# Performance work log

Hardware: AMD Instinct MI355X
Metric: run time of the kernel (lower is better)

Reference implementation:

```python
import jax, jax.numpy as jnp
import numpy as np


def setup_inputs() -> dict:
    key = jax.random.key(0)
    k1, k2, k3, k4 = jax.random.split(key, 4)
    B, N, F_in, F_out = 8, 2048, 256, 128
    h = jax.random.normal(k1, (B, N, F_in), dtype=jnp.float32)
    # fc: Linear(in_features, out_features, bias=False); store as [F_in, F_out]
    W_fc = jax.random.normal(k2, (F_in, F_out), dtype=jnp.float32) * (1.0 / np.sqrt(F_in))
    # attn_fc: Linear(2*F_out, 1, bias=False) -> split into the two additive halves
    a_i = jax.random.normal(k3, (F_out,), dtype=jnp.float32) * (1.0 / np.sqrt(2 * F_out))
    a_j = jax.random.normal(k4, (F_out,), dtype=jnp.float32) * (1.0 / np.sqrt(2 * F_out))
    return {"h": h, "W_fc": W_fc, "a_i": a_i, "a_j": a_j}


def reference(h, W_fc, a_i, a_j):
    # Wh: [B, N, F_out]
    Wh = jnp.einsum("bnf,fo->bno", h, W_fc)
    # attn_fc(cat([Wh_i, Wh_j])) is linear, so it decomposes additively:
    # e[b,i,j] = <Wh[b,i], a_i> + <Wh[b,j], a_j>  -- same math, no N^2*2F tensor
    s_i = Wh @ a_i  # [B, N]
    s_j = Wh @ a_j  # [B, N]
    e = s_i[:, :, None] + s_j[:, None, :]  # [B, N, N]
    alpha = jax.nn.softmax(jax.nn.leaky_relu(e, negative_slope=0.01), axis=-1)
    h_prime = jnp.einsum("bij,bjo->bio", alpha, Wh)  # [B, N, F_out]
    return h_prime
```

## Files before the change

kernel.cpp:

```cpp
#include <hip/hip_runtime.h>
#include <hip/hip_bf16.h>

#define BATCH 8
#define NN 2048
#define FIN 256
#define FOUT 128
#define ROWS (BATCH*NN)
#define NP1 (NN+1)
#define SEGS 128
#define SLEN (NN/SEGS)

typedef __attribute__((ext_vector_type(8))) __bf16 bf16x8;
typedef __attribute__((ext_vector_type(4))) float f32x4;
typedef __attribute__((ext_vector_type(8))) unsigned short ushort8_t;

__device__ __forceinline__ unsigned pack2(float a, float b){
  __hip_bfloat16 x = __float2bfloat16(a), y = __float2bfloat16(b);
  unsigned short ux = *(unsigned short*)&x, uy = *(unsigned short*)&y;
  return ((unsigned)uy << 16) | (unsigned)ux;
}
__device__ __forceinline__ float lo2f(unsigned u){ union{unsigned v;float f;}c; c.v = u << 16; return c.f; }
__device__ __forceinline__ float hi2f(unsigned u){ union{unsigned v;float f;}c; c.v = u & 0xffff0000u; return c.f; }

__device__ __forceinline__ void bsplit(float x, unsigned short& hu, unsigned short& lu){
  __hip_bfloat16 hb = __float2bfloat16(x);
  hu = *(unsigned short*)&hb;
  union{unsigned u; float f;} hf; hf.u = (unsigned)hu << 16;
  __hip_bfloat16 lb = __float2bfloat16(x - hf.f);
  lu = *(unsigned short*)&lb;
}

__global__ __launch_bounds__(256) void k_wsplit(const float* __restrict__ W,
                                                unsigned short* __restrict__ Wth,
                                                unsigned short* __restrict__ Wtl){
  const int gid = blockIdx.x * 256 + threadIdx.x;
  const int k = gid >> 5, c4 = (gid & 31) * 4;
  float4 v = *(const float4*)&W[(size_t)k * FOUT + c4];
  float xs[4] = {v.x, v.y, v.z, v.w};
  #pragma unroll
  for (int i = 0; i < 4; i++){
    unsigned short hu, lu;
    bsplit(xs[i], hu, lu);
    Wth[(size_t)(c4 + i) * FIN + k] = hu;
    Wtl[(size_t)(c4 + i) * FIN + k] = lu;
  }
}

__global__ __launch_bounds__(256) void k_gemm(const float* __restrict__ h,
                                              const unsigned short* __restrict__ Wth,
                                              const unsigned short* __restrict__ Wtl,
                                              const float* __restrict__ ai,
                                              const float* __restrict__ aj,
                                              float* __restrict__ Wh,
                                              float* __restrict__ sI,
                                              float* __restrict__ sJ){
  __shared__ unsigned short Ah[32*40], Al[32*40];
  __shared__ unsigned short Bh[128*40], Bl[128*40];
  __shared__ float spI[2][32], spJ[2][32];
  const int t = threadIdx.x;
  const int rbase = blockIdx.x * 32;
  const int w = t >> 6, l = t & 63;
  const int g = w & 1, cg = w >> 1;
  const int lr = l & 15, lq = l >> 4;
  const int sar = t >> 3, sak = (t & 7) * 4;
  const int sbc = t >> 1, sbh = (t & 1) * 16;

  f32x4 acc[4];
  #pragma unroll
  for (int ct = 0; ct < 4; ct++) acc[ct] = (f32x4){0.f, 0.f, 0.f, 0.f};

  for (int k0 = 0; k0 < FIN; k0 += 32){
    {
      float4 hv = *(const float4*)&h[(size_t)(rbase + sar) * FIN + k0 + sak];
      float xs[4] = {hv.x, hv.y, hv.z, hv.w};
      ushort4 hh, ll;
      unsigned short hu, lu;
      bsplit(xs[0], hu, lu); hh.x = hu; ll.x = lu;
      bsplit(xs[1], hu, lu); hh.y = hu; ll.y = lu;
      bsplit(xs[2], hu, lu); hh.z = hu; ll.z = lu;
      bsplit(xs[3], hu, lu); hh.w = hu; ll.w = lu;
      *(ushort4*)&Ah[sar * 40 + sak] = hh;
      *(ushort4*)&Al[sar * 40 + sak] = ll;
    }
    {
      const size_t gb = (size_t)sbc * FIN + k0 + sbh;
      ushort8_t b0 = *(const ushort8_t*)&Wth[gb];
      ushort8_t b1 = *(const ushort8_t*)&Wth[gb + 8];
      ushort8_t c0 = *(const ushort8_t*)&Wtl[gb];
      ushort8_t c1 = *(const ushort8_t*)&Wtl[gb + 8];
      *(ushort8_t*)&Bh[sbc * 40 + sbh]     = b0;
      *(ushort8_t*)&Bh[sbc * 40 + sbh + 8] = b1;
      *(ushort8_t*)&Bl[sbc * 40 + sbh]     = c0;
      *(ushort8_t*)&Bl[sbc * 40 + sbh + 8] = c1;
    }
    __syncthreads();
    const bf16x8 avh = __builtin_bit_cast(bf16x8, *(const ushort8_t*)&Ah[(g*16 + lr)*40 + lq*8]);
    const bf16x8 avl = __builtin_bit_cast(bf16x8, *(const ushort8_t*)&Al[(g*16 + lr)*40 + lq*8]);
    #pragma unroll
    for (int ct = 0; ct < 4; ct++){
      const int col = cg*64 + ct*16 + lr;
      const bf16x8 bvh = __builtin_bit_cast(bf16x8, *(const ushort8_t*)&Bh[col*40 + lq*8]);
      const bf16x8 bvl = __builtin_bit_cast(bf16x8, *(const ushort8_t*)&Bl[col*40 + lq*8]);
      acc[ct] = __builtin_amdgcn_mfma_f32_16x16x32_bf16(avh, bvh, acc[ct], 0, 0, 0);
      acc[ct] = __builtin_amdgcn_mfma_f32_16x16x32_bf16(avh, bvl, acc[ct], 0, 0, 0);
      acc[ct] = __builtin_amdgcn_mfma_f32_16x16x32_bf16(avl, bvh, acc[ct], 0, 0, 0);
    }
    __syncthreads();
  }
  float pi[4] = {0.f,0.f,0.f,0.f}, pj[4] = {0.f,0.f,0.f,0.f};
  #pragma unroll
  for (int ct = 0; ct < 4; ct++){
    const int col = cg*64 + ct*16 + lr;
    const float fai = ai[col], faj = aj[col];
    #pragma unroll
    for (int q = 0; q < 4; q++){
      const float val = acc[ct][q];
      Wh[(size_t)(rbase + g*16 + lq*4 + q) * FOUT + col] = val;
      pi[q] = fmaf(val, fai, pi[q]);
      pj[q] = fmaf(val, faj, pj[q]);
    }
  }
  #pragma unroll
  for (int q = 0; q < 4; q++){
    #pragma unroll
    for (int m = 1; m < 16; m <<= 1){
      pi[q] += __shfl_xor(pi[q], m);
      pj[q] += __shfl_xor(pj[q], m);
    }
  }
  if (lr == 0){
    #pragma unroll
    for (int q = 0; q < 4; q++){
      spI[cg][g*16 + lq*4 + q] = pi[q];
      spJ[cg][g*16 + lq*4 + q] = pj[q];
    }
  }
  __syncthreads();
  if (t < 32){
    sI[rbase + t] = spI[0][t] + spI[1][t];
    sJ[rbase + t] = spJ[0][t] + spJ[1][t];
  }
}

__global__ __launch_bounds__(256) void k_rank_scatter(const float* __restrict__ sJ,
                                                      float* __restrict__ sortedS,
                                                      int* __restrict__ perm,
                                                      float2* __restrict__ e12g){
  const int b = blockIdx.x >> 6;
  const int jc = blockIdx.x & 63;
  __shared__ float v[NN];
  __shared__ int partial[8][32];
  const int t = threadIdx.x;
  const float* sj = sJ + b * NN;
  #pragma unroll
  for (int u = 0; u < 2; u++)
    ((float4*)v)[t + u * 256] = ((const float4*)sj)[t + u * 256];
  const int jj = t & 31, qq = t >> 5;
  const int j = jc * 32 + jj;
  const float x = sj[j];
  __syncthreads();
  const int q0 = qq * 256;
  int r = 0;
  #pragma unroll 8
  for (int q4 = 0; q4 < 64; q4++){
    const int q = q0 + q4 * 4;
    float4 y = *(const float4*)&v[q];
    r += (y.x < x) || (y.x == x && (q + 0) < j);
    r += (y.y < x) || (y.y == x && (q + 1) < j);
    r += (y.z < x) || (y.z == x && (q + 2) < j);
    r += (y.w < x) || (y.w == x && (q + 3) < j);
  }
  partial[qq][jj] = r;
  __syncthreads();
  if (t < 32){
    int R = 0;
    #pragma unroll
    for (int q8 = 0; q8 < 8; q8++) R += partial[q8][t];
    const int myj = jc * 32 + t;
    const float xx = v[myj];
    sortedS[b * NN + R] = xx;
    perm[b * NN + R] = myj;
    e12g[b * NN + R] = make_float2(expf(xx), expf(0.01f * xx));
  }
}

__global__ __launch_bounds__(512) void k_fuseout(const float* __restrict__ sortedS,
                                                 const float* __restrict__ sI,
                                                 const float2* __restrict__ e12g,
                                                 const float* __restrict__ Wh,
                                                 const int* __restrict__ perm,
                                                 float* __restrict__ out){
  __shared__ float    ssL[NN];
  __shared__ float2   abL[NP1];
  __shared__ unsigned PL[NP1][4];
  __shared__ float p1[SEGS][4], p2[SEGS][4];
  __shared__ float p1s[SEGS], p2s[SEGS];
  const int bc = blockIdx.x;
  const int b = bc >> 5;
  const int og = bc & 31;
  const int t = threadIdx.x;
  const int ol = t & 3;
  const int o = og * 4 + ol;
  const int seg = t >> 2;
  const int r0 = seg * SLEN;

  const float* ssg = sortedS + b * NN;
  #pragma unroll
  for (int u = 0; u < 4; u++) ssL[t + u * 512] = ssg[t + u * 512];

  const int*    pm  = perm + b * NN;
  const float2* e12 = e12g + b * NN;
  const float*  whb = Wh + (size_t)b * NN * FOUT;
  float w[SLEN], ex[SLEN], ey[SLEN];
  float t1 = 0.f, t2 = 0.f, s1 = 0.f, s2 = 0.f;
  #pragma unroll
  for (int r = 0; r < SLEN; r++){
    w[r] = whb[(size_t)pm[r0 + r] * FOUT + o];
    const float2 u = e12[r0 + r];
    ex[r] = u.x; ey[r] = u.y;
    t1 = fmaf(u.x, w[r], t1);
    t2 = fmaf(u.y, w[r], t2);
    s1 += u.x; s2 += u.y;
  }
  p1[seg][ol] = t1; p2[seg][ol] = t2;
  if (ol == 0){ p1s[seg] = s1; p2s[seg] = s2; }
  __syncthreads();
  #pragma unroll
  for (int d = 1; d < SEGS; d <<= 1){
    const float u1 = (seg >= d) ? p1[seg - d][ol] : 0.f;
    const float u2 = (seg >= d) ? p2[seg - d][ol] : 0.f;
    const float v1 = (ol == 0 && seg >= d) ? p1s[seg - d] : 0.f;
    const float v2 = (ol == 0 && seg >= d) ? p2s[seg - d] : 0.f;
    __syncthreads();
    if (seg >= d){
      p1[seg][ol] += u1; p2[seg][ol] += u2;
      if (ol == 0){ p1s[seg] += v1; p2s[seg] += v2; }
    }
    __syncthreads();
  }
  float acc1 = p1[seg][ol] - t1;
  float acc2 = p2[seg][ol] - t2;
  if (seg == 0){
    PL[0][ol] = 0u;
    if (ol == 0) abL[0] = make_float2(0.f, 0.f);
  }
  {
    float offs1 = 0.f, offs2 = 0.f;
    if (ol == 0){ offs1 = p1s[seg] - s1; offs2 = p2s[seg] - s2; }
    float run1 = 0.f, run2 = 0.f;
    #pragma unroll
    for (int r = 0; r < SLEN; r++){
      acc1 = fmaf(ex[r], w[r], acc1);
      acc2 = fmaf(ey[r], w[r], acc2);
      PL[r0 + r + 1][ol] = pack2(acc1, acc2);
      if (ol == 0){
        run1 += ex[r]; run2 += ey[r];
        abL[r0 + r + 1] = make_float2(offs1 + run1, offs2 + run2);
      }
    }
  }
  __syncthreads();
  const int tg = t >> 2;
  float sv[16];
  #pragma unroll
  for (int u = 0; u < 16; u++) sv[u] = sI[b * NN + tg + u * 128];
  int lo[16], hi[16];
  #pragma unroll
  for (int u = 0; u < 16; u++){ lo[u] = 0; hi[u] = NN; }
  #pragma unroll
  for (int step = 0; step < 11; step++){
    float mv[16]; int mid[16];
    #pragma unroll
    for (int u = 0; u < 16; u++){
      mid[u] = (lo[u] + hi[u]) >> 1;
      mv[u] = ssL[mid[u]];
    }
    #pragma unroll
    for (int u = 0; u < 16; u++){
      if (mv[u] <= -sv[u]) lo[u] = mid[u] + 1; else hi[u] = mid[u];
    }
  }
  const float2 vT = abL[NN];
  const unsigned uTp = PL[NN][ol];
  #pragma unroll
  for (int u = 0; u < 16; u++){
    const int row = tg + u * 128;
    const int k = lo[u];
    const float s = sv[u];
    const float w1 = expf(s), w2 = expf(0.01f * s);
    const float2 vk = abL[k];
    const float inv = 1.0f / (w1 * (vT.x - vk.x) + w2 * vk.y);
    const unsigned uk = PL[k][ol];
    const float num = w1 * (lo2f(uTp) - lo2f(uk)) + w2 * hi2f(uk);
    out[(size_t)(b * NN + row) * FOUT + o] = num * inv;
  }
}

extern "C" void kernel_launch(void* const* d_in, const int* in_sizes, int n_in,
                              void* d_out, int out_size, void* d_ws, size_t ws_size,
                              hipStream_t stream){
  const float* h  = (const float*)d_in[0];
  const float* W  = (const float*)d_in[1];
  const float* ai = (const float*)d_in[2];
  const float* aj = (const float*)d_in[3];
  float* out = (float*)d_out;

  char* ws = (char*)d_ws;
  size_t off = 0;
  auto alloc = [&](size_t bytes) -> void* {
    void* p = ws + off;
    off += (bytes + 255) & ~(size_t)255;
    return p;
  };
  float*          Wh   = (float*)   alloc((size_t)ROWS * FOUT * 4);
  float*          sI   = (float*)   alloc((size_t)ROWS * 4);
  float*          sJ   = (float*)   alloc((size_t)ROWS * 4);
  float*          sortedS = (float*)alloc((size_t)BATCH * NN * 4);
  int*            perm = (int*)     alloc((size_t)BATCH * NN * 4);
  float2*         e12  = (float2*)  alloc((size_t)BATCH * NN * 8);
  unsigned short* Wth  = (unsigned short*)alloc((size_t)FOUT * FIN * 2);
  unsigned short* Wtl  = (unsigned short*)alloc((size_t)FOUT * FIN * 2);

  k_wsplit      <<<32, 256, 0, stream>>>(W, Wth, Wtl);
  k_gemm        <<<ROWS / 32, 256, 0, stream>>>(h, Wth, Wtl, ai, aj, Wh, sI, sJ);
  k_rank_scatter<<<BATCH * 64, 256, 0, stream>>>(sJ, sortedS, perm, e12);
  k_fuseout     <<<BATCH * 32, 512, 0, stream>>>(sortedS, sI, e12, Wh, perm, out);
}
```

Before: 116.3 us.

## Store Wh in per-column-group layout and use wavefront shuffle scan

The GEMM kernel now writes Wh in a [B][32 groups][N][4] layout, so each fuseout block's permuted gathers read contiguous 16-byte rows instead of strided 4-byte values spread across 512-byte rows. The segment prefix scan in fuseout, previously a 7-step shared-memory Hillis-Steele scan with two barriers per step, becomes an intra-wavefront shuffle-up scan followed by one barrier and a serial add of the per-wave totals. The goal is fewer wasted cache-line fetches and fewer block-wide synchronisations. In exchange, the GEMM epilogue stores become more scattered.

```diff
diff --git a/kernel.cpp b/kernel.cpp
--- a/kernel.cpp
+++ b/kernel.cpp
@@ -59,6 +59,8 @@
   __shared__ float spI[2][32], spJ[2][32];
   const int t = threadIdx.x;
   const int rbase = blockIdx.x * 32;
+  const int b = rbase >> 11;
+  const int brow0 = rbase & (NN - 1);
   const int w = t >> 6, l = t & 63;
   const int g = w & 1, cg = w >> 1;
   const int lr = l & 15, lq = l >> 4;
@@ -111,11 +113,13 @@
   #pragma unroll
   for (int ct = 0; ct < 4; ct++){
     const int col = cg*64 + ct*16 + lr;
+    const int og = col >> 2, ol2 = col & 3;
     const float fai = ai[col], faj = aj[col];
+    const size_t obase = ((size_t)(b * 32 + og) * NN + brow0 + g*16 + lq*4) * 4 + ol2;
     #pragma unroll
     for (int q = 0; q < 4; q++){
       const float val = acc[ct][q];
-      Wh[(size_t)(rbase + g*16 + lq*4 + q) * FOUT + col] = val;
+      Wh[obase + (size_t)q * 4] = val;
       pi[q] = fmaf(val, fai, pi[q]);
       pj[q] = fmaf(val, faj, pj[q]);
     }
@@ -193,16 +197,15 @@
   __shared__ float    ssL[NN];
   __shared__ float2   abL[NP1];
   __shared__ unsigned PL[NP1][4];
-  __shared__ float p1[SEGS][4], p2[SEGS][4];
-  __shared__ float p1s[SEGS], p2s[SEGS];
+  __shared__ float wtP1[8][4], wtP2[8][4], wtS1[8], wtS2[8];
   const int bc = blockIdx.x;
   const int b = bc >> 5;
   const int og = bc & 31;
   const int t = threadIdx.x;
   const int ol = t & 3;
-  const int o = og * 4 + ol;
   const int seg = t >> 2;
   const int r0 = seg * SLEN;
+  const int wv = t >> 6, wl = t & 63;
 
   const float* ssg = sortedS + b * NN;
   #pragma unroll
@@ -210,43 +213,45 @@
 
   const int*    pm  = perm + b * NN;
   const float2* e12 = e12g + b * NN;
-  const float*  whb = Wh + (size_t)b * NN * FOUT;
+  const float*  whb = Wh + (size_t)(b * 32 + og) * NN * 4;
   float w[SLEN], ex[SLEN], ey[SLEN];
   float t1 = 0.f, t2 = 0.f, s1 = 0.f, s2 = 0.f;
   #pragma unroll
   for (int r = 0; r < SLEN; r++){
-    w[r] = whb[(size_t)pm[r0 + r] * FOUT + o];
+    w[r] = whb[(size_t)pm[r0 + r] * 4 + ol];
     const float2 u = e12[r0 + r];
     ex[r] = u.x; ey[r] = u.y;
     t1 = fmaf(u.x, w[r], t1);
     t2 = fmaf(u.y, w[r], t2);
     s1 += u.x; s2 += u.y;
   }
-  p1[seg][ol] = t1; p2[seg][ol] = t2;
-  if (ol == 0){ p1s[seg] = s1; p2s[seg] = s2; }
-  __syncthreads();
-  #pragma unroll
-  for (int d = 1; d < SEGS; d <<= 1){
-    const float u1 = (seg >= d) ? p1[seg - d][ol] : 0.f;
-    const float u2 = (seg >= d) ? p2[seg - d][ol] : 0.f;
-    const float v1 = (ol == 0 && seg >= d) ? p1s[seg - d] : 0.f;
-    const float v2 = (ol == 0 && seg >= d) ? p2s[seg - d] : 0.f;
-    __syncthreads();
-    if (seg >= d){
-      p1[seg][ol] += u1; p2[seg][ol] += u2;
-      if (ol == 0){ p1s[seg] += v1; p2s[seg] += v2; }
-    }
-    __syncthreads();
-  }
-  float acc1 = p1[seg][ol] - t1;
-  float acc2 = p2[seg][ol] - t2;
+  float c1 = t1, c2 = t2, cs1 = s1, cs2 = s2;
+  #pragma unroll
+  for (int d = 1; d < 16; d <<= 1){
+    const float u1 = __shfl_up(c1, d * 4);
+    const float u2 = __shfl_up(c2, d * 4);
+    const float u3 = __shfl_up(cs1, d * 4);
+    const float u4 = __shfl_up(cs2, d * 4);
+    if ((wl >> 2) >= d){ c1 += u1; c2 += u2; cs1 += u3; cs2 += u4; }
+  }
+  if ((wl >> 2) == 15){
+    wtP1[wv][ol] = c1; wtP2[wv][ol] = c2;
+    if (ol == 0){ wtS1[wv] = cs1; wtS2[wv] = cs2; }
+  }
+  __syncthreads();
+  for (int ww = 0; ww < wv; ww++){
+    c1 += wtP1[ww][ol]; c2 += wtP2[ww][ol];
+    cs1 += wtS1[ww];    cs2 += wtS2[ww];
+  }
+  float acc1 = c1 - t1;
+  float acc2 = c2 - t2;
   if (seg == 0){
     PL[0][ol] = 0u;
     if (ol == 0) abL[0] = make_float2(0.f, 0.f);
   }
   {
     float offs1 = 0.f, offs2 = 0.f;
-    if (ol == 0){ offs1 = p1s[seg] - s1; offs2 = p2s[seg] - s2; }
+    if (ol == 0){ offs1 = cs1 - s1; offs2 = cs2 - s2; }
     float run1 = 0.f, run2 = 0.f;
     #pragma unroll
     for (int r = 0; r < SLEN; r++){
@@ -292,7 +297,7 @@
     const float inv = 1.0f / (w1 * (vT.x - vk.x) + w2 * vk.y);
     const unsigned uk = PL[k][ol];
     const float num = w1 * (lo2f(uTp) - lo2f(uk)) + w2 * hi2f(uk);
-    out[(size_t)(b * NN + row) * FOUT + o] = num * inv;
+    out[(size_t)(b * NN + row) * FOUT + og * 4 + ol] = num * inv;
   }
 }
 
```

After: 109.8 us. 5.6% less time.
